# Kernel tuning notes

Hardware: AMD Instinct MI355X
Metric: run time of the kernel (lower is better)

The kernel has to match this reference:

```python
import jax, jax.numpy as jnp
import numpy as np

TOP_K = 2

def moe_linear(x, router_w, experts_w):
    # x: [T, din]; router_w: [din, E]; experts_w: [E, din, dout]
    T = x.shape[0]
    E = experts_w.shape[0]
    probs = jax.nn.softmax(x @ router_w, axis=-1)            # [T, E]
    topv, topi = jax.lax.top_k(probs, TOP_K)                 # [T, k]
    topv = topv / jnp.sum(topv, axis=-1, keepdims=True)      # renormalize over selected experts
    w = jnp.zeros((T, E), x.dtype).at[jnp.arange(T)[:, None], topi].set(topv)  # dense routing weights
    y = jnp.zeros((T, experts_w.shape[2]), x.dtype)
    for e in range(E):  # small fixed expert loop; avoids [T,E,dout] intermediate
        y = y + w[:, e:e+1] * (x @ experts_w[e])
    return y

def setup_inputs() -> dict:
    key = jax.random.key(0)
    ks = jax.random.split(key, 7)
    B, S, H, I, E = 4, 2048, 1024, 3584, 8
    sH, sI = 1.0 / np.sqrt(H), 1.0 / np.sqrt(I)
    return {
        "hidden_state": jax.random.normal(ks[0], (B, S, H), jnp.float32),
        "gate_router": jax.random.normal(ks[1], (H, E), jnp.float32) * sH,
        "gate_experts": jax.random.normal(ks[2], (E, H, I), jnp.float32) * sH,
        "up_router": jax.random.normal(ks[3], (H, E), jnp.float32) * sH,
        "up_experts": jax.random.normal(ks[4], (E, H, I), jnp.float32) * sH,
        "down_router": jax.random.normal(ks[5], (I, E), jnp.float32) * sI,
        "down_experts": jax.random.normal(ks[6], (E, I, H), jnp.float32) * sI,
    }

def reference(hidden_state, gate_router, gate_experts, up_router, up_experts, down_router, down_experts):
    B, S, H = hidden_state.shape
    x = hidden_state.reshape(B * S, H)
    g = moe_linear(x, gate_router, gate_experts)             # [T, I]
    u = moe_linear(x, up_router, up_experts)                 # [T, I]
    h = jax.nn.silu(g) * u                                   # SwiGLU
    y = moe_linear(h, down_router, down_experts)             # [T, H]
    return y.reshape(B, S, H)
```

## Files before the change

kernel.cpp:

```cpp
#include <hip/hip_runtime.h>
#include <stdint.h>
#include <stdio.h>

#define T_TOK 8192
#define HDIM  1024
#define IDIM  3584
#define NEXP  8
#define NPAIR (T_TOK*2)
#define BM 128
#define BN 128
#define BK 32
#define NTK  96

typedef float          f32x4 __attribute__((ext_vector_type(4)));
typedef short          s16x8 __attribute__((ext_vector_type(8)));
typedef unsigned short u16x4 __attribute__((ext_vector_type(4)));
typedef unsigned short u16x8 __attribute__((ext_vector_type(8)));

__device__ __forceinline__ unsigned short f2bf_rne(float f) {
  unsigned u = __float_as_uint(f);
  u += 0x7FFFu + ((u >> 16) & 1u);
  return (unsigned short)(u >> 16);
}
__device__ __forceinline__ float bf2f(unsigned short h) {
  return __uint_as_float(((unsigned)h) << 16);
}

__device__ __forceinline__ void gld16(const void* gsrc, void* ldst) {
  typedef const unsigned int __attribute__((address_space(1))) GU;
  typedef unsigned int       __attribute__((address_space(3))) LU;
  __builtin_amdgcn_global_load_lds((GU*)(unsigned long long)gsrc,
                                   (LU*)(unsigned int)(unsigned long long)ldst,
                                   16, 0, 0);
}

__global__ void split_hilo(const float* __restrict__ in,
                           unsigned short* __restrict__ hi,
                           unsigned short* __restrict__ lo, int n4) {
  int i = blockIdx.x*blockDim.x + threadIdx.x;
  int s = gridDim.x*blockDim.x;
  for (; i < n4; i += s) {
    f32x4 v = ((const f32x4*)in)[i];
    u16x4 h, l;
#pragma unroll
    for (int j = 0; j < 4; j++) {
      float f = v[j];
      unsigned short hb = f2bf_rne(f);
      h[j] = hb;
      l[j] = f2bf_rne(f - bf2f(hb));
    }
    ((u16x4*)hi)[i] = h;
    ((u16x4*)lo)[i] = l;
  }
}

__global__ void transpose_split(const float* __restrict__ W,
                                unsigned short* __restrict__ hi,
                                unsigned short* __restrict__ lo,
                                int K, int N) {
  __shared__ float tile[32][33];
  long base = (long)blockIdx.z * K * N;
  int n0 = blockIdx.x*32, k0 = blockIdx.y*32;
  int tx = threadIdx.x, ty = threadIdx.y;
#pragma unroll
  for (int r = 0; r < 4; r++)
    tile[ty+8*r][tx] = W[base + (long)(k0+ty+8*r)*N + n0 + tx];
  __syncthreads();
#pragma unroll
  for (int r = 0; r < 4; r++) {
    float f = tile[tx][ty+8*r];
    long o = base + (long)(n0+ty+8*r)*K + k0 + tx;
    unsigned short hb = f2bf_rne(f);
    hi[o] = hb;
    if (lo) lo[o] = f2bf_rne(f - bf2f(hb));
  }
}

__device__ __forceinline__ void top2_write(const float* acc, int t,
                                           int* __restrict__ topi,
                                           float* __restrict__ topw) {
  int i0 = 0; float l0 = acc[0];
#pragma unroll
  for (int e = 1; e < NEXP; e++) if (acc[e] > l0) { l0 = acc[e]; i0 = e; }
  int i1 = -1; float l1 = -3.4e38f;
#pragma unroll
  for (int e = 0; e < NEXP; e++) if (e != i0 && acc[e] > l1) { l1 = acc[e]; i1 = e; }
  float w0 = 1.f/(1.f + expf(l1 - l0));
  float w1 = 1.f/(1.f + expf(l0 - l1));
  topi[2*t]   = i0; topi[2*t+1] = i1;
  topw[2*t]   = w0; topw[2*t+1] = w1;
}

__global__ __launch_bounds__(256) void router2_topk(
    const float* __restrict__ X,
    const float* __restrict__ RWg, const float* __restrict__ RWu,
    int* __restrict__ tig, float* __restrict__ twg,
    int* __restrict__ tiu, float* __restrict__ twu) {
  int lane = threadIdx.x & 63;
  int t = blockIdx.x*4 + (threadIdx.x>>6);
  const f32x4* xr = (const f32x4*)(X + (long)t*HDIM);
  float ag[NEXP], au[NEXP];
#pragma unroll
  for (int e = 0; e < NEXP; e++) { ag[e] = 0.f; au[e] = 0.f; }
#pragma unroll
  for (int it = 0; it < HDIM/4/64; it++) {
    int c4 = it*64 + lane;
    f32x4 xv = xr[c4];
#pragma unroll
    for (int j = 0; j < 4; j++) {
      const float* wg = RWg + (long)(c4*4+j)*NEXP;
      const float* wu = RWu + (long)(c4*4+j)*NEXP;
#pragma unroll
      for (int e = 0; e < NEXP; e++) { ag[e] += xv[j]*wg[e]; au[e] += xv[j]*wu[e]; }
    }
  }
#pragma unroll
  for (int e = 0; e < NEXP; e++) {
    float vg = ag[e], vu = au[e];
#pragma unroll
    for (int o = 1; o < 64; o <<= 1) { vg += __shfl_xor(vg, o); vu += __shfl_xor(vu, o); }
    ag[e] = vg; au[e] = vu;
  }
  if (lane == 0) { top2_write(ag, t, tig, twg); top2_write(au, t, tiu, twu); }
}

__global__ __launch_bounds__(256) void build_perm(const int* __restrict__ topi,
                                                  const float* __restrict__ topw,
                                                  int* __restrict__ offs,
                                                  int* __restrict__ ptok,
                                                  float* __restrict__ pw) {
  int e = blockIdx.x;
  int tid = threadIdx.x, lane = tid & 63, wv = tid >> 6;
  __shared__ int cnt[NEXP];
  __shared__ int wsum[4];
  if (tid < NEXP) cnt[tid] = 0;
  __syncthreads();
  for (int p = tid; p < NPAIR; p += 256) atomicAdd(&cnt[topi[p]], 1);
  __syncthreads();
  int base = 0;
#pragma unroll
  for (int e2 = 0; e2 < NEXP; e2++) if (e2 < e) base += cnt[e2];
  if (tid == 0) { offs[e] = base; if (e == NEXP-1) offs[NEXP] = base + cnt[e]; }
  for (int p0 = 0; p0 < NPAIR; p0 += 256) {
    int p = p0 + tid;
    bool m = (topi[p] == e);
    unsigned long long b = __ballot(m);
    int lp = __popcll(b & ((1ull << lane) - 1ull));
    if (lane == 0) wsum[wv] = __popcll(b);
    __syncthreads();
    int woff = 0;
#pragma unroll
    for (int w2 = 0; w2 < 4; w2++) if (w2 < wv) woff += wsum[w2];
    int tot = wsum[0] + wsum[1] + wsum[2] + wsum[3];
    if (m) { int dst = base + woff + lp; ptok[dst] = p >> 1; pw[dst] = topw[p]; }
    base += tot;
    __syncthreads();
  }
}

__global__ __launch_bounds__(512, 2) void moe_gemm3_8p(
    const unsigned short* __restrict__ Ahi, const unsigned short* __restrict__ Alo,
    const unsigned short* __restrict__ Bhi, const unsigned short* __restrict__ Blo,
    const int* __restrict__ offs, const int* __restrict__ ptok,
    const float* __restrict__ pw, float* __restrict__ out)
{
  const int e = blockIdx.z;
  const int beg = offs[e];
  const int cnt = offs[e+1] - beg;
  const int m0 = blockIdx.y * 256;
  if (m0 >= cnt) return;
  const int n0 = blockIdx.x * 256;

  __shared__ unsigned short AsL[3][256*32];
  __shared__ unsigned short BsL[3][256*32];
  __shared__ int   stok[256];
  __shared__ float swt[256];

  const int tid = threadIdx.x, lane = tid & 63, wv = tid >> 6;
  if (tid < 256) {
    int i = m0 + tid;
    stok[tid] = ptok[beg + (i < cnt ? i : 0)];
    swt[tid]  = (i < cnt) ? pw[beg + i] : 0.f;
  }
  __syncthreads();

  const int srow = lane >> 2;
  const int lc   = ((lane & 3) - ((lane >> 3) & 3)) & 3;
  const long aoff0 = (long)stok[wv*32 +      srow]*HDIM + lc*8;
  const long aoff1 = (long)stok[wv*32 + 16 + srow]*HDIM + lc*8;
  const long boff0 = ((long)e*IDIM + n0 + wv*32 +      srow)*HDIM + lc*8;
  const long boff1 = ((long)e*IDIM + n0 + wv*32 + 16 + srow)*HDIM + lc*8;
  const int adst0 = (wv*32     )*32;
  const int adst1 = (wv*32 + 16)*32;

#define STAGE_A(buf, kt) do {                                              \
    int s_ = (kt) >> 5; int kl_ = ((kt) & 31) * 32;                        \
    const unsigned short* ap_ = (s_ == 1) ? Alo : Ahi;                     \
    gld16(ap_ + aoff0 + kl_, &AsL[buf][adst0]);                            \
    gld16(ap_ + aoff1 + kl_, &AsL[buf][adst1]);                            \
  } while (0)
#define STAGE_B(buf, kt) do {                                              \
    int s_ = (kt) >> 5; int kl_ = ((kt) & 31) * 32;                        \
    const unsigned short* bp_ = (s_ == 2) ? Blo : Bhi;                     \
    gld16(bp_ + boff0 + kl_, &BsL[buf][adst0]);                            \
    gld16(bp_ + boff1 + kl_, &BsL[buf][adst1]);                            \
  } while (0)

  const int fl = lane & 15, fg = lane >> 4;
  const int pks = (((fg + (fl >> 1)) & 3) << 3);
  const int wm = wv >> 2, wn = wv & 3;
  const int arow = wm * 128;
  const int bcol = wn * 64;

  f32x4 acc[8][4];
#pragma unroll
  for (int m = 0; m < 8; m++)
#pragma unroll
    for (int n = 0; n < 4; n++) acc[m][n] = {0.f, 0.f, 0.f, 0.f};

  STAGE_A(0, 0); STAGE_B(0, 0);
  STAGE_A(1, 1); STAGE_B(1, 1);
  asm volatile("s_waitcnt vmcnt(0)" ::: "memory");
  __syncthreads();

  int buf = 0, nbuf = 2;
  for (int kt = 0; kt < NTK; ++kt) {
    const bool st = (kt + 2 < NTK);
    s16x8 bhf[4], ahf[4];

    if (st) STAGE_A(nbuf, kt + 2);
#pragma unroll
    for (int n = 0; n < 4; n++)
      bhf[n] = *(const s16x8*)&BsL[buf][(bcol + n*16 + fl)*32 + pks];
#pragma unroll
    for (int i = 0; i < 4; i++)
      ahf[i] = *(const s16x8*)&AsL[buf][(arow + i*16 + fl)*32 + pks];
    __builtin_amdgcn_s_setprio(1);
#pragma unroll
    for (int i = 0; i < 4; i++)
#pragma unroll
      for (int n = 0; n < 4; n++)
        acc[i][n] = __builtin_amdgcn_mfma_f32_16x16x32_bf16(ahf[i], bhf[n], acc[i][n], 0,0,0);
    __builtin_amdgcn_s_setprio(0);

    if (st) STAGE_B(nbuf, kt + 2);
#pragma unroll
    for (int i = 0; i < 4; i++)
      ahf[i] = *(const s16x8*)&AsL[buf][(arow + (4+i)*16 + fl)*32 + pks];
    __builtin_amdgcn_s_setprio(1);
#pragma unroll
    for (int i = 0; i < 4; i++)
#pragma unroll
      for (int n = 0; n < 4; n++)
        acc[4+i][n] = __builtin_amdgcn_mfma_f32_16x16x32_bf16(ahf[i], bhf[n], acc[4+i][n], 0,0,0);
    __builtin_amdgcn_s_setprio(0);

    if (st) asm volatile("s_waitcnt vmcnt(4)" ::: "memory");
    else    asm volatile("s_waitcnt vmcnt(0)" ::: "memory");
    __builtin_amdgcn_s_barrier();
    __builtin_amdgcn_sched_barrier(0);

    buf  = (buf  == 2) ? 0 : buf + 1;
    nbuf = (nbuf == 2) ? 0 : nbuf + 1;
  }
#undef STAGE_A
#undef STAGE_B

#pragma unroll
  for (int m = 0; m < 8; m++)
#pragma unroll
    for (int r = 0; r < 4; r++) {
      int lrow = arow + m*16 + fg*4 + r;
      if (m0 + lrow < cnt) {
        float wt = swt[lrow];
        long ob = (long)stok[lrow]*IDIM + n0 + bcol + fl;
#pragma unroll
        for (int n = 0; n < 4; n++)
          atomicAdd(&out[ob + n*16], wt * acc[m][n][r]);
      }
    }
}

__global__ __launch_bounds__(256) void swiglu_router(
    float* __restrict__ g, const float* __restrict__ u,
    const float* __restrict__ RW,
    int* __restrict__ topi, float* __restrict__ topw) {
  int lane = threadIdx.x & 63;
  int t = blockIdx.x*4 + (threadIdx.x>>6);
  f32x4*       gr = (f32x4*)(g + (long)t*IDIM);
  const f32x4* ur = (const f32x4*)(u + (long)t*IDIM);
  float acc[NEXP];
#pragma unroll
  for (int e = 0; e < NEXP; e++) acc[e] = 0.f;
#pragma unroll
  for (int it = 0; it < IDIM/4/64; it++) {
    int c4 = it*64 + lane;
    f32x4 gv = gr[c4], uv = ur[c4], hv;
#pragma unroll
    for (int j = 0; j < 4; j++) {
      float x = gv[j];
      hv[j] = x * uv[j] / (1.f + expf(-x));
    }
    gr[c4] = hv;
#pragma unroll
    for (int j = 0; j < 4; j++) {
      const float* wr = RW + (long)(c4*4+j)*NEXP;
#pragma unroll
      for (int e = 0; e < NEXP; e++) acc[e] += hv[j]*wr[e];
    }
  }
#pragma unroll
  for (int e = 0; e < NEXP; e++) {
    float v = acc[e];
#pragma unroll
    for (int o = 1; o < 64; o <<= 1) v += __shfl_xor(v, o);
    acc[e] = v;
  }
  if (lane == 0) top2_write(acc, t, topi, topw);
}

__global__ __launch_bounds__(256) void moe_gemm_down(
    const float* __restrict__ Hf, const unsigned short* __restrict__ Bw,
    const int* __restrict__ offs, const int* __restrict__ ptok,
    const float* __restrict__ pw, float* __restrict__ out)
{
  const int K = IDIM, N = HDIM;
  const int e = blockIdx.z;
  const int beg = offs[e];
  const int cnt = offs[e+1] - beg;
  const int m0 = blockIdx.y * BM;
  if (m0 >= cnt) return;
  const int n0 = blockIdx.x * BN;

  __shared__ unsigned short Ah[BM*BK], Bh[BN*BK];
  __shared__ int   stok[BM];
  __shared__ float swt[BM];

  const int tid = threadIdx.x, lane = tid & 63, wv = tid >> 6;
  if (tid < BM) {
    int i = m0 + tid;
    stok[tid] = ptok[beg + (i < cnt ? i : 0)];
    swt[tid]  = (i < cnt) ? pw[beg + i] : 0.f;
  }
  __syncthreads();

  const int arw = tid >> 1, half = tid & 1;
  const float* asrc = Hf + (long)stok[arw]*K + half*16;
  const int awoff = arw*BK + half*16;

  const int srow = lane >> 2, scol = (lane & 3)*8;
  const int r0 = (wv*2+0)*16 + srow, r1 = (wv*2+1)*16 + srow;
  const long b0 = ((long)e*N + n0 + r0)*K + scol;
  const long b1 = ((long)e*N + n0 + r1)*K + scol;
  unsigned short* dB0 = &Bh[(wv*2+0)*16*BK];
  unsigned short* dB1 = &Bh[(wv*2+1)*16*BK];

  f32x4 zero = {0.f,0.f,0.f,0.f};
  f32x4 acc[4][4];
#pragma unroll
  for (int i = 0; i < 4; i++)
#pragma unroll
    for (int j = 0; j < 4; j++) acc[i][j] = zero;

  const int arow = (wv>>1)*64, bcol = (wv&1)*64;
  const int fl = lane & 15, fg = lane >> 4;

  f32x4 p0, p1, p2, p3;
#define LOADA(kk) do {                        \
    p0 = ((const f32x4*)(asrc + (kk)))[0];    \
    p1 = ((const f32x4*)(asrc + (kk)))[1];    \
    p2 = ((const f32x4*)(asrc + (kk)))[2];    \
    p3 = ((const f32x4*)(asrc + (kk)))[3];    \
  } while (0)

  LOADA(0);

  for (int kk = 0; kk < K; kk += BK) {
    __syncthreads();
    gld16(Bw + b0 + kk, dB0);
    gld16(Bw + b1 + kk, dB1);
    u16x8 ha, hb2;
    ha[0]=f2bf_rne(p0[0]); ha[1]=f2bf_rne(p0[1]); ha[2]=f2bf_rne(p0[2]); ha[3]=f2bf_rne(p0[3]);
    ha[4]=f2bf_rne(p1[0]); ha[5]=f2bf_rne(p1[1]); ha[6]=f2bf_rne(p1[2]); ha[7]=f2bf_rne(p1[3]);
    hb2[0]=f2bf_rne(p2[0]); hb2[1]=f2bf_rne(p2[1]); hb2[2]=f2bf_rne(p2[2]); hb2[3]=f2bf_rne(p2[3]);
    hb2[4]=f2bf_rne(p3[0]); hb2[5]=f2bf_rne(p3[1]); hb2[6]=f2bf_rne(p3[2]); hb2[7]=f2bf_rne(p3[3]);
    *(u16x8*)&Ah[awoff]   = ha;
    *(u16x8*)&Ah[awoff+8] = hb2;
    asm volatile("s_waitcnt vmcnt(0)" ::: "memory");
    __syncthreads();

    if (kk + BK < K) LOADA(kk + BK);

    s16x8 ahf[4], bhf[4];
#pragma unroll
    for (int i = 0; i < 4; i++) {
      ahf[i] = *(const s16x8*)&Ah[(arow + i*16 + fl)*BK + fg*8];
      bhf[i] = *(const s16x8*)&Bh[(bcol + i*16 + fl)*BK + fg*8];
    }
#pragma unroll
    for (int i = 0; i < 4; i++)
#pragma unroll
      for (int j = 0; j < 4; j++)
        acc[i][j] = __builtin_amdgcn_mfma_f32_16x16x32_bf16(ahf[i], bhf[j], acc[i][j], 0,0,0);
  }
#undef LOADA

#pragma unroll
  for (int i = 0; i < 4; i++)
#pragma unroll
    for (int r = 0; r < 4; r++) {
      int lrow = arow + i*16 + fg*4 + r;
      if (m0 + lrow < cnt) {
        float wt = swt[lrow];
        long ob = (long)stok[lrow]*N + n0 + bcol + fl;
#pragma unroll
        for (int j = 0; j < 4; j++)
          atomicAdd(&out[ob + j*16], wt * acc[i][j][r]);
      }
    }
}

extern "C" void kernel_launch(void* const* d_in, const int* in_sizes, int n_in,
                              void* d_out, int out_size, void* d_ws, size_t ws_size,
                              hipStream_t stream)
{
  (void)in_sizes; (void)n_in;
  const float* x   = (const float*)d_in[0];
  const float* grt = (const float*)d_in[1];
  const float* gex = (const float*)d_in[2];
  const float* urt = (const float*)d_in[3];
  const float* uex = (const float*)d_in[4];
  const float* drt = (const float*)d_in[5];
  const float* dex = (const float*)d_in[6];
  float* out = (float*)d_out;

  char* base = (char*)d_ws;
  size_t off = 0;
  auto alloc = [&](size_t b) -> void* {
    void* r = base + off;
    off = (off + b + 255) & ~(size_t)255;
    return r;
  };
  const size_t szXH = (size_t)T_TOK*HDIM*2;
  const size_t szW  = (size_t)NEXP*HDIM*IDIM*2;
  const size_t szGI = (size_t)T_TOK*IDIM*4;

  unsigned short* xhi   = (unsigned short*)alloc(szXH);
  unsigned short* xlo   = (unsigned short*)alloc(szXH);
  unsigned short* wg_hi = (unsigned short*)alloc(szW);
  unsigned short* wg_lo = (unsigned short*)alloc(szW);
  unsigned short* wu_hi = (unsigned short*)alloc(szW);
  unsigned short* wu_lo = (unsigned short*)alloc(szW);
  float* gbuf = (float*)alloc(szGI);
  int*   topi_g = (int*)alloc(NPAIR*4);  float* topw_g = (float*)alloc(NPAIR*4);
  int*   topi_u = (int*)alloc(NPAIR*4);  float* topw_u = (float*)alloc(NPAIR*4);
  int*   topi_d = (int*)alloc(NPAIR*4);  float* topw_d = (float*)alloc(NPAIR*4);
  int* offs_g = (int*)alloc(64);
  int* offs_u = (int*)alloc(64);
  int* offs_d = (int*)alloc(64);
  int*   ptok_g = (int*)alloc(NPAIR*4);  float* pw_g = (float*)alloc(NPAIR*4);
  int*   ptok_u = (int*)alloc(NPAIR*4);  float* pw_u = (float*)alloc(NPAIR*4);
  int*   ptok_d = (int*)alloc(NPAIR*4);  float* pw_d = (float*)alloc(NPAIR*4);

  float*          ubuf  = (float*)wg_hi;
  unsigned short* wd_hi = wu_hi;

  if (off > ws_size) {
    fprintf(stderr, "[moe] ws too small: need %zu bytes, have %zu\n", off, ws_size);
    hipMemsetAsync(d_out, 0, (size_t)out_size*sizeof(float), stream);
    return;
  }

  hipMemsetAsync(gbuf, 0, szGI, stream);
  hipMemsetAsync(d_out, 0, (size_t)out_size*sizeof(float), stream);

  split_hilo<<<2048, 256, 0, stream>>>(x, xhi, xlo, T_TOK*HDIM/4);
  transpose_split<<<dim3(IDIM/32, HDIM/32, NEXP), dim3(32,8), 0, stream>>>(gex, wg_hi, wg_lo, HDIM, IDIM);
  transpose_split<<<dim3(IDIM/32, HDIM/32, NEXP), dim3(32,8), 0, stream>>>(uex, wu_hi, wu_lo, HDIM, IDIM);
  router2_topk<<<T_TOK/4, 256, 0, stream>>>(x, grt, urt, topi_g, topw_g, topi_u, topw_u);
  build_perm<<<NEXP, 256, 0, stream>>>(topi_g, topw_g, offs_g, ptok_g, pw_g);
  build_perm<<<NEXP, 256, 0, stream>>>(topi_u, topw_u, offs_u, ptok_u, pw_u);

  moe_gemm3_8p<<<dim3(IDIM/256, 64, NEXP), 512, 0, stream>>>(
      xhi, xlo, wg_hi, wg_lo, offs_g, ptok_g, pw_g, gbuf);

  hipMemsetAsync(ubuf, 0, szGI, stream);
  moe_gemm3_8p<<<dim3(IDIM/256, 64, NEXP), 512, 0, stream>>>(
      xhi, xlo, wu_hi, wu_lo, offs_u, ptok_u, pw_u, ubuf);

  transpose_split<<<dim3(HDIM/32, IDIM/32, NEXP), dim3(32,8), 0, stream>>>(dex, wd_hi, nullptr, IDIM, HDIM);

  swiglu_router<<<T_TOK/4, 256, 0, stream>>>(gbuf, ubuf, drt, topi_d, topw_d);
  build_perm<<<NEXP, 256, 0, stream>>>(topi_d, topw_d, offs_d, ptok_d, pw_d);

  moe_gemm_down<<<dim3(HDIM/BN, T_TOK/BM, NEXP), 256, 0, stream>>>(
      gbuf, wd_hi, offs_d, ptok_d, pw_d, out);
}
```

Before: 1.843 ms.

## Fuse hi/lo split-bf16 passes into one K loop with double-buffered tiles

The gate/up expert GEMM used to run the three split-precision products (hi·hi, lo·hi, hi·lo) as three sequential sweeps over K, 96 triple-buffered steps in total. It now loads the hi and lo halves of each K tile together into a double buffer and issues all three MFMA products per tile. This reuses A fragments across products and cuts the number of loop barriers. The grid's M dimension is halved to 32, enough to cover the largest possible per-expert token count. The cost is a larger shared-memory footprint, more live fragment registers, and a dropped minimum-occupancy hint. The explicit vmcnt waits are also gone, so the async LDS loads now depend on plain __syncthreads for ordering.

```diff
diff --git a/kernel.cpp b/kernel.cpp
--- a/kernel.cpp
+++ b/kernel.cpp
@@ -10,7 +10,6 @@
 #define BM 128
 #define BN 128
 #define BK 32
-#define NTK  96
 
 typedef float          f32x4 __attribute__((ext_vector_type(4)));
 typedef short          s16x8 __attribute__((ext_vector_type(8)));
@@ -158,7 +157,7 @@
   }
 }
 
-__global__ __launch_bounds__(512, 2) void moe_gemm3_8p(
+__global__ __launch_bounds__(512) void moe_gemm3_mt(
     const unsigned short* __restrict__ Ahi, const unsigned short* __restrict__ Alo,
     const unsigned short* __restrict__ Bhi, const unsigned short* __restrict__ Blo,
     const int* __restrict__ offs, const int* __restrict__ ptok,
@@ -171,8 +170,8 @@
   if (m0 >= cnt) return;
   const int n0 = blockIdx.x * 256;
 
-  __shared__ unsigned short AsL[3][256*32];
-  __shared__ unsigned short BsL[3][256*32];
+  __shared__ unsigned short As[2][2][256*32];
+  __shared__ unsigned short Bs[2][2][256*32];
   __shared__ int   stok[256];
   __shared__ float swt[256];
 
@@ -190,20 +189,22 @@
   const long aoff1 = (long)stok[wv*32 + 16 + srow]*HDIM + lc*8;
   const long boff0 = ((long)e*IDIM + n0 + wv*32 +      srow)*HDIM + lc*8;
   const long boff1 = ((long)e*IDIM + n0 + wv*32 + 16 + srow)*HDIM + lc*8;
-  const int adst0 = (wv*32     )*32;
-  const int adst1 = (wv*32 + 16)*32;
-
-#define STAGE_A(buf, kt) do {                                              \
-    int s_ = (kt) >> 5; int kl_ = ((kt) & 31) * 32;                        \
-    const unsigned short* ap_ = (s_ == 1) ? Alo : Ahi;                     \
-    gld16(ap_ + aoff0 + kl_, &AsL[buf][adst0]);                            \
-    gld16(ap_ + aoff1 + kl_, &AsL[buf][adst1]);                            \
+  const int dst0 = (wv*32     )*32;
+  const int dst1 = (wv*32 + 16)*32;
+
+#define STAGE_A(buf, kk) do {                                   \
+    int kl_ = (kk)*32;                                          \
+    gld16(Ahi + aoff0 + kl_, &As[buf][0][dst0]);                \
+    gld16(Ahi + aoff1 + kl_, &As[buf][0][dst1]);                \
+    gld16(Alo + aoff0 + kl_, &As[buf][1][dst0]);                \
+    gld16(Alo + aoff1 + kl_, &As[buf][1][dst1]);                \
   } while (0)
-#define STAGE_B(buf, kt) do {                                              \
-    int s_ = (kt) >> 5; int kl_ = ((kt) & 31) * 32;                        \
-    const unsigned short* bp_ = (s_ == 2) ? Blo : Bhi;                     \
-    gld16(bp_ + boff0 + kl_, &BsL[buf][adst0]);                            \
-    gld16(bp_ + boff1 + kl_, &BsL[buf][adst1]);                            \
+#define STAGE_B(buf, kk) do {                                   \
+    int kl_ = (kk)*32;                                          \
+    gld16(Bhi + boff0 + kl_, &Bs[buf][0][dst0]);                \
+    gld16(Bhi + boff1 + kl_, &Bs[buf][0][dst1]);                \
+    gld16(Blo + boff0 + kl_, &Bs[buf][1][dst0]);                \
+    gld16(Blo + boff1 + kl_, &Bs[buf][1][dst1]);                \
   } while (0)
 
   const int fl = lane & 15, fg = lane >> 4;
@@ -218,50 +219,58 @@
 #pragma unroll
     for (int n = 0; n < 4; n++) acc[m][n] = {0.f, 0.f, 0.f, 0.f};
 
-  STAGE_A(0, 0); STAGE_B(0, 0);
-  STAGE_A(1, 1); STAGE_B(1, 1);
-  asm volatile("s_waitcnt vmcnt(0)" ::: "memory");
+  STAGE_A(0, 0);
+  STAGE_B(0, 0);
   __syncthreads();
 
-  int buf = 0, nbuf = 2;
-  for (int kt = 0; kt < NTK; ++kt) {
-    const bool st = (kt + 2 < NTK);
-    s16x8 bhf[4], ahf[4];
-
-    if (st) STAGE_A(nbuf, kt + 2);
+  int cur = 0;
+  for (int kt = 0; kt < HDIM/BK; ++kt) {
+    const bool st = (kt + 1 < HDIM/BK);
+    s16x8 ahf[8], bf4[4];
+
+    if (st) STAGE_A(cur^1, kt + 1);
 #pragma unroll
     for (int n = 0; n < 4; n++)
-      bhf[n] = *(const s16x8*)&BsL[buf][(bcol + n*16 + fl)*32 + pks];
-#pragma unroll
-    for (int i = 0; i < 4; i++)
-      ahf[i] = *(const s16x8*)&AsL[buf][(arow + i*16 + fl)*32 + pks];
+      bf4[n] = *(const s16x8*)&Bs[cur][0][(bcol + n*16 + fl)*32 + pks];
+#pragma unroll
+    for (int i = 0; i < 8; i++)
+      ahf[i] = *(const s16x8*)&As[cur][0][(arow + i*16 + fl)*32 + pks];
     __builtin_amdgcn_s_setprio(1);
 #pragma unroll
-    for (int i = 0; i < 4; i++)
+    for (int i = 0; i < 8; i++)
 #pragma unroll
       for (int n = 0; n < 4; n++)
-        acc[i][n] = __builtin_amdgcn_mfma_f32_16x16x32_bf16(ahf[i], bhf[n], acc[i][n], 0,0,0);
+        acc[i][n] = __builtin_amdgcn_mfma_f32_16x16x32_bf16(ahf[i], bf4[n], acc[i][n], 0,0,0);
     __builtin_amdgcn_s_setprio(0);
 
-    if (st) STAGE_B(nbuf, kt + 2);
-#pragma unroll
-    for (int i = 0; i < 4; i++)
-      ahf[i] = *(const s16x8*)&AsL[buf][(arow + (4+i)*16 + fl)*32 + pks];
+    if (st) STAGE_B(cur^1, kt + 1);
+#pragma unroll
+    for (int n = 0; n < 4; n++)
+      bf4[n] = *(const s16x8*)&Bs[cur][1][(bcol + n*16 + fl)*32 + pks];
     __builtin_amdgcn_s_setprio(1);
 #pragma unroll
-    for (int i = 0; i < 4; i++)
+    for (int i = 0; i < 8; i++)
 #pragma unroll
       for (int n = 0; n < 4; n++)
-        acc[4+i][n] = __builtin_amdgcn_mfma_f32_16x16x32_bf16(ahf[i], bhf[n], acc[4+i][n], 0,0,0);
+        acc[i][n] = __builtin_amdgcn_mfma_f32_16x16x32_bf16(ahf[i], bf4[n], acc[i][n], 0,0,0);
     __builtin_amdgcn_s_setprio(0);
 
-    if (st) asm volatile("s_waitcnt vmcnt(4)" ::: "memory");
-    else    asm volatile("s_waitcnt vmcnt(0)" ::: "memory");
-    __builtin_amdgcn_s_barrier();
-    __builtin_amdgcn_sched_barrier(0);
-
-    buf  = (buf  == 2) ? 0 : buf + 1;
-    nbuf = (nbuf == 2) ? 0 : nbuf + 1;
+#pragma unroll
+    for (int i = 0; i < 8; i++)
+      ahf[i] = *(const s16x8*)&As[cur][1][(arow + i*16 + fl)*32 + pks];
+#pragma unroll
+    for (int n = 0; n < 4; n++)
+      bf4[n] = *(const s16x8*)&Bs[cur][0][(bcol + n*16 + fl)*32 + pks];
+    __builtin_amdgcn_s_setprio(1);
+#pragma unroll
+    for (int i = 0; i < 8; i++)
+#pragma unroll
+      for (int n = 0; n < 4; n++)
+        acc[i][n] = __builtin_amdgcn_mfma_f32_16x16x32_bf16(ahf[i], bf4[n], acc[i][n], 0,0,0);
+    __builtin_amdgcn_s_setprio(0);
+
+    __syncthreads();
+    cur ^= 1;
   }
 #undef STAGE_A
 #undef STAGE_B
@@ -481,11 +490,11 @@
   build_perm<<<NEXP, 256, 0, stream>>>(topi_g, topw_g, offs_g, ptok_g, pw_g);
   build_perm<<<NEXP, 256, 0, stream>>>(topi_u, topw_u, offs_u, ptok_u, pw_u);
 
-  moe_gemm3_8p<<<dim3(IDIM/256, 64, NEXP), 512, 0, stream>>>(
+  moe_gemm3_mt<<<dim3(IDIM/256, 32, NEXP), 512, 0, stream>>>(
       xhi, xlo, wg_hi, wg_lo, offs_g, ptok_g, pw_g, gbuf);
 
   hipMemsetAsync(ubuf, 0, szGI, stream);
-  moe_gemm3_8p<<<dim3(IDIM/256, 64, NEXP), 512, 0, stream>>>(
+  moe_gemm3_mt<<<dim3(IDIM/256, 32, NEXP), 512, 0, stream>>>(
       xhi, xlo, wu_hi, wu_lo, offs_u, ptok_u, pw_u, ubuf);
 
   transpose_split<<<dim3(HDIM/32, IDIM/32, NEXP), dim3(32,8), 0, stream>>>(dex, wd_hi, nullptr, IDIM, HDIM);
```

Result: faster. 1.732 ms (-6.1%).

## Restructure split-bf16 expert GEMM to fuse hi/lo passes per K tile

Applied to the files above, without the earlier changes.

The gate/up expert GEMM used to walk K three times (hi*hi, lo*hi, hi*lo), one 32-wide segment per iteration, with a 256x256 block tile. It now stages both hi and lo halves of A and B for each K tile and issues all three MFMA products in one iteration. That cuts the loop to a third as many iterations and barriers, and reuses the hi fragments across two products. The block tile shrinks to 256x128, with each wave owning 64x64 instead of 128x64, and the grid's M dimension is halved. In exchange, A tiles are re-read from global memory by twice as many N blocks, and each wave has lower register-level reuse.

```diff
diff --git a/kernel.cpp b/kernel.cpp
--- a/kernel.cpp
+++ b/kernel.cpp
@@ -10,7 +10,6 @@
 #define BM 128
 #define BN 128
 #define BK 32
-#define NTK  96
 
 typedef float          f32x4 __attribute__((ext_vector_type(4)));
 typedef short          s16x8 __attribute__((ext_vector_type(8)));
@@ -158,21 +157,22 @@
   }
 }
 
-__global__ __launch_bounds__(512, 2) void moe_gemm3_8p(
+__global__ __launch_bounds__(512) void moe_gemm3_cv(
     const unsigned short* __restrict__ Ahi, const unsigned short* __restrict__ Alo,
     const unsigned short* __restrict__ Bhi, const unsigned short* __restrict__ Blo,
     const int* __restrict__ offs, const int* __restrict__ ptok,
     const float* __restrict__ pw, float* __restrict__ out)
 {
+  const int NT = HDIM/BK;
   const int e = blockIdx.z;
   const int beg = offs[e];
   const int cnt = offs[e+1] - beg;
   const int m0 = blockIdx.y * 256;
   if (m0 >= cnt) return;
-  const int n0 = blockIdx.x * 256;
-
-  __shared__ unsigned short AsL[3][256*32];
-  __shared__ unsigned short BsL[3][256*32];
+  const int n0 = blockIdx.x * 128;
+
+  __shared__ unsigned short As[3][2][256*32];
+  __shared__ unsigned short Bs[3][2][128*32];
   __shared__ int   stok[256];
   __shared__ float swt[256];
 
@@ -188,86 +188,93 @@
   const int lc   = ((lane & 3) - ((lane >> 3) & 3)) & 3;
   const long aoff0 = (long)stok[wv*32 +      srow]*HDIM + lc*8;
   const long aoff1 = (long)stok[wv*32 + 16 + srow]*HDIM + lc*8;
-  const long boff0 = ((long)e*IDIM + n0 + wv*32 +      srow)*HDIM + lc*8;
-  const long boff1 = ((long)e*IDIM + n0 + wv*32 + 16 + srow)*HDIM + lc*8;
-  const int adst0 = (wv*32     )*32;
-  const int adst1 = (wv*32 + 16)*32;
-
-#define STAGE_A(buf, kt) do {                                              \
-    int s_ = (kt) >> 5; int kl_ = ((kt) & 31) * 32;                        \
-    const unsigned short* ap_ = (s_ == 1) ? Alo : Ahi;                     \
-    gld16(ap_ + aoff0 + kl_, &AsL[buf][adst0]);                            \
-    gld16(ap_ + aoff1 + kl_, &AsL[buf][adst1]);                            \
-  } while (0)
-#define STAGE_B(buf, kt) do {                                              \
-    int s_ = (kt) >> 5; int kl_ = ((kt) & 31) * 32;                        \
-    const unsigned short* bp_ = (s_ == 2) ? Blo : Bhi;                     \
-    gld16(bp_ + boff0 + kl_, &BsL[buf][adst0]);                            \
-    gld16(bp_ + boff1 + kl_, &BsL[buf][adst1]);                            \
+  const long boff  = ((long)e*IDIM + n0 + wv*16 + srow)*HDIM + lc*8;
+  const int dstA0 = (wv*32     )*32;
+  const int dstA1 = (wv*32 + 16)*32;
+  const int dstB  = (wv*16     )*32;
+
+#define STAGE(buf, kk) do {                                  \
+    int kl_ = (kk)*32;                                       \
+    gld16(Ahi + aoff0 + kl_, &As[buf][0][dstA0]);            \
+    gld16(Ahi + aoff1 + kl_, &As[buf][0][dstA1]);            \
+    gld16(Alo + aoff0 + kl_, &As[buf][1][dstA0]);            \
+    gld16(Alo + aoff1 + kl_, &As[buf][1][dstA1]);            \
+    gld16(Bhi + boff  + kl_, &Bs[buf][0][dstB]);             \
+    gld16(Blo + boff  + kl_, &Bs[buf][1][dstB]);             \
   } while (0)
 
   const int fl = lane & 15, fg = lane >> 4;
   const int pks = (((fg + (fl >> 1)) & 3) << 3);
-  const int wm = wv >> 2, wn = wv & 3;
-  const int arow = wm * 128;
+  const int wm = wv >> 1, wn = wv & 1;
+  const int arow = wm * 64;
   const int bcol = wn * 64;
 
-  f32x4 acc[8][4];
-#pragma unroll
-  for (int m = 0; m < 8; m++)
+  f32x4 acc[4][4];
+#pragma unroll
+  for (int m = 0; m < 4; m++)
 #pragma unroll
     for (int n = 0; n < 4; n++) acc[m][n] = {0.f, 0.f, 0.f, 0.f};
 
-  STAGE_A(0, 0); STAGE_B(0, 0);
-  STAGE_A(1, 1); STAGE_B(1, 1);
-  asm volatile("s_waitcnt vmcnt(0)" ::: "memory");
-  __syncthreads();
-
-  int buf = 0, nbuf = 2;
-  for (int kt = 0; kt < NTK; ++kt) {
-    const bool st = (kt + 2 < NTK);
-    s16x8 bhf[4], ahf[4];
-
-    if (st) STAGE_A(nbuf, kt + 2);
+  STAGE(0, 0);
+  STAGE(1, 1);
+  asm volatile("s_waitcnt vmcnt(6)" ::: "memory");
+  __builtin_amdgcn_s_barrier();
+  __builtin_amdgcn_sched_barrier(0);
+
+  int cur = 0;
+  for (int kt = 0; kt < NT; ++kt) {
+    const int nxt2 = (cur + 2 >= 3) ? cur - 1 : cur + 2;
+    const bool st = (kt + 2 < NT);
+    if (st) STAGE(nxt2, kt + 2);
+
+    s16x8 ahi[4], bhi[4], bx[4];
+#pragma unroll
+    for (int i = 0; i < 4; i++)
+      ahi[i] = *(const s16x8*)&As[cur][0][(arow + i*16 + fl)*32 + pks];
 #pragma unroll
     for (int n = 0; n < 4; n++)
-      bhf[n] = *(const s16x8*)&BsL[buf][(bcol + n*16 + fl)*32 + pks];
+      bhi[n] = *(const s16x8*)&Bs[cur][0][(bcol + n*16 + fl)*32 + pks];
+    __builtin_amdgcn_s_setprio(1);
 #pragma unroll
     for (int i = 0; i < 4; i++)
-      ahf[i] = *(const s16x8*)&AsL[buf][(arow + i*16 + fl)*32 + pks];
+#pragma unroll
+      for (int n = 0; n < 4; n++)
+        acc[i][n] = __builtin_amdgcn_mfma_f32_16x16x32_bf16(ahi[i], bhi[n], acc[i][n], 0,0,0);
+    __builtin_amdgcn_s_setprio(0);
+
+#pragma unroll
+    for (int n = 0; n < 4; n++)
+      bx[n] = *(const s16x8*)&Bs[cur][1][(bcol + n*16 + fl)*32 + pks];
     __builtin_amdgcn_s_setprio(1);
 #pragma unroll
     for (int i = 0; i < 4; i++)
 #pragma unroll
       for (int n = 0; n < 4; n++)
-        acc[i][n] = __builtin_amdgcn_mfma_f32_16x16x32_bf16(ahf[i], bhf[n], acc[i][n], 0,0,0);
+        acc[i][n] = __builtin_amdgcn_mfma_f32_16x16x32_bf16(ahi[i], bx[n], acc[i][n], 0,0,0);
     __builtin_amdgcn_s_setprio(0);
 
-    if (st) STAGE_B(nbuf, kt + 2);
 #pragma unroll
     for (int i = 0; i < 4; i++)
-      ahf[i] = *(const s16x8*)&AsL[buf][(arow + (4+i)*16 + fl)*32 + pks];
+      ahi[i] = *(const s16x8*)&As[cur][1][(arow + i*16 + fl)*32 + pks];
     __builtin_amdgcn_s_setprio(1);
 #pragma unroll
     for (int i = 0; i < 4; i++)
 #pragma unroll
       for (int n = 0; n < 4; n++)
-        acc[4+i][n] = __builtin_amdgcn_mfma_f32_16x16x32_bf16(ahf[i], bhf[n], acc[4+i][n], 0,0,0);
+        acc[i][n] = __builtin_amdgcn_mfma_f32_16x16x32_bf16(ahi[i], bhi[n], acc[i][n], 0,0,0);
     __builtin_amdgcn_s_setprio(0);
 
-    if (st) asm volatile("s_waitcnt vmcnt(4)" ::: "memory");
+    if (st) asm volatile("s_waitcnt vmcnt(6)" ::: "memory");
     else    asm volatile("s_waitcnt vmcnt(0)" ::: "memory");
     __builtin_amdgcn_s_barrier();
     __builtin_amdgcn_sched_barrier(0);
 
-    buf  = (buf  == 2) ? 0 : buf + 1;
-    nbuf = (nbuf == 2) ? 0 : nbuf + 1;
-  }
-#undef STAGE_A
-#undef STAGE_B
-
-#pragma unroll
-  for (int m = 0; m < 8; m++)
+    cur = (cur + 1 >= 3) ? 0 : cur + 1;
+  }
+#undef STAGE
+
+#pragma unroll
+  for (int m = 0; m < 4; m++)
 #pragma unroll
     for (int r = 0; r < 4; r++) {
       int lrow = arow + m*16 + fg*4 + r;
@@ -481,11 +488,11 @@
   build_perm<<<NEXP, 256, 0, stream>>>(topi_g, topw_g, offs_g, ptok_g, pw_g);
   build_perm<<<NEXP, 256, 0, stream>>>(topi_u, topw_u, offs_u, ptok_u, pw_u);
 
-  moe_gemm3_8p<<<dim3(IDIM/256, 64, NEXP), 512, 0, stream>>>(
+  moe_gemm3_cv<<<dim3(IDIM/128, 32, NEXP), 512, 0, stream>>>(
       xhi, xlo, wg_hi, wg_lo, offs_g, ptok_g, pw_g, gbuf);
 
   hipMemsetAsync(ubuf, 0, szGI, stream);
-  moe_gemm3_8p<<<dim3(IDIM/256, 64, NEXP), 512, 0, stream>>>(
+  moe_gemm3_cv<<<dim3(IDIM/128, 32, NEXP), 512, 0, stream>>>(
       xhi, xlo, wu_hi, wu_lo, offs_u, ptok_u, pw_u, ubuf);
 
   transpose_split<<<dim3(HDIM/32, IDIM/32, NEXP), dim3(32,8), 0, stream>>>(dex, wd_hi, nullptr, IDIM, HDIM);
```

Result: faster. 1.750 ms (-5.1%).
